# Optimization experiments

Hardware: AMD Instinct MI355X
Metric: run time of the kernel (lower is better)

## Reference

```python
import jax, jax.numpy as jnp
import numpy as np

EPS = 1e-5

def _layernorm(x, g, b):
    mu = jnp.mean(x, axis=-1, keepdims=True)
    var = jnp.mean(jnp.square(x - mu), axis=-1, keepdims=True)
    return (x - mu) * jax.lax.rsqrt(var + EPS) * g + b

def setup_inputs() -> dict:
    key = jax.random.key(0)
    ks = jax.random.split(key, 4)
    E, B, D, H = 8, 131072, 128, 128
    features = jax.random.normal(ks[0], (E, B, D), dtype=jnp.float32)
    gate_w1 = jax.random.normal(ks[1], (E * D, H), dtype=jnp.float32) * (1.0 / np.sqrt(E * D))
    gate_b1 = jnp.zeros((H,), dtype=jnp.float32)
    ln1_g = jnp.ones((H,), dtype=jnp.float32)
    ln1_b = jnp.zeros((H,), dtype=jnp.float32)
    gate_w2 = jax.random.normal(ks[2], (H, E), dtype=jnp.float32) * (1.0 / np.sqrt(H))
    gate_b2 = jnp.zeros((E,), dtype=jnp.float32)
    out_g = jnp.ones((D,), dtype=jnp.float32)
    out_b = jnp.zeros((D,), dtype=jnp.float32)
    return {"features": features, "gate_w1": gate_w1, "gate_b1": gate_b1,
            "ln1_g": ln1_g, "ln1_b": ln1_b, "gate_w2": gate_w2, "gate_b2": gate_b2,
            "out_g": out_g, "out_b": out_b}

def reference(features, gate_w1, gate_b1, ln1_g, ln1_b, gate_w2, gate_b2, out_g, out_b):
    # features: [E, B, D]
    E, B, D = features.shape
    # concat teacher features per sample -> [B, E*D]
    concat = jnp.transpose(features, (1, 0, 2)).reshape(B, E * D)
    h = concat @ gate_w1 + gate_b1                       # [B, 128]
    h = jax.nn.gelu(h, approximate=False)                # torch nn.GELU default = exact
    h = _layernorm(h, ln1_g, ln1_b)
    logits = h @ gate_w2 + gate_b2                       # [B, E]
    scores = jax.nn.softmax(logits, axis=-1)             # [B, E]
    # per-expert scalar weight then LayerNorm over D
    weighted = scores.T[:, :, None] * features           # [E, B, D]
    out = _layernorm(weighted, out_g, out_b)             # [E, B, D]
    return out
```

## Files before the change

### kernel.cpp

```cpp
#include <hip/hip_runtime.h>
#include <hip/hip_bf16.h>

#define B_N   131072
#define E_N   8
#define D_N   128
#define H_N   128
#define K_N   1024
#define MBLK  32
#define NTHR  512

typedef __attribute__((ext_vector_type(8))) short bf16x8;
typedef __attribute__((ext_vector_type(4))) float f32x4;
typedef __attribute__((ext_vector_type(4))) unsigned short u16x4;

__device__ __forceinline__ unsigned short f2bf(float f) {
    union { float f; unsigned int i; } c; c.f = f;
    unsigned int x = c.i;
    return (unsigned short)((x + 0x7fffu + ((x >> 16) & 1u)) >> 16);
}
__device__ __forceinline__ float bf2f(unsigned short u) {
    union { unsigned int i; float f; } c; c.i = ((unsigned int)u) << 16; return c.f;
}

__global__ void prep_w1_frags(const float* __restrict__ w1,
                              unsigned short* __restrict__ frag) {
    int t    = blockIdx.x * blockDim.x + threadIdx.x;
    int lane = t & 63;
    int fgi  = t >> 6;
    int kst  = fgi >> 3;
    int nt   = fgi & 7;
    int n    = nt * 16 + (lane & 15);
    int k0   = kst * 32 + (lane >> 4) * 8;
    bf16x8 v;
    #pragma unroll
    for (int j = 0; j < 8; ++j)
        v[j] = (short)f2bf(w1[(k0 + j) * H_N + n]);
    *reinterpret_cast<bf16x8*>(frag + (size_t)t * 8) = v;
}

__global__ __launch_bounds__(NTHR, 4)
void moe_fused(const float* __restrict__ feats,
               const unsigned short* __restrict__ w1frag,
               const float* __restrict__ gate_b1,
               const float* __restrict__ ln1_g,
               const float* __restrict__ ln1_b,
               const float* __restrict__ gate_w2,
               const float* __restrict__ gate_b2,
               const float* __restrict__ out_g,
               const float* __restrict__ out_b,
               float* __restrict__ out)
{
    __shared__ __attribute__((aligned(16))) unsigned short featS[MBLK * K_N];
    __shared__ __attribute__((aligned(16))) unsigned short hSb[MBLK * 136];
    __shared__ float scoreS[MBLK * E_N];

    const int tid = threadIdx.x;
    const int b0  = blockIdx.x * MBLK;

    #pragma unroll
    for (int i = 0; i < 2; ++i) {
        const int f  = tid + i * NTHR;
        const int m  = f >> 5;
        const int dq = f & 31;
        f32x4 v0 = reinterpret_cast<const f32x4*>(feats + ((size_t)0 * B_N + b0) * D_N)[f];
        f32x4 v1 = reinterpret_cast<const f32x4*>(feats + ((size_t)1 * B_N + b0) * D_N)[f];
        f32x4 v2 = reinterpret_cast<const f32x4*>(feats + ((size_t)2 * B_N + b0) * D_N)[f];
        f32x4 v3 = reinterpret_cast<const f32x4*>(feats + ((size_t)3 * B_N + b0) * D_N)[f];
        f32x4 v4 = reinterpret_cast<const f32x4*>(feats + ((size_t)4 * B_N + b0) * D_N)[f];
        f32x4 v5 = reinterpret_cast<const f32x4*>(feats + ((size_t)5 * B_N + b0) * D_N)[f];
        f32x4 v6 = reinterpret_cast<const f32x4*>(feats + ((size_t)6 * B_N + b0) * D_N)[f];
        f32x4 v7 = reinterpret_cast<const f32x4*>(feats + ((size_t)7 * B_N + b0) * D_N)[f];
        const int sw = (m & 7);
        const int mb = m * K_N;
        #pragma unroll
        for (int e = 0; e < 8; ++e) {
            f32x4 v = (e == 0) ? v0 : (e == 1) ? v1 : (e == 2) ? v2 : (e == 3) ? v3
                    : (e == 4) ? v4 : (e == 5) ? v5 : (e == 6) ? v6 : v7;
            int k    = e * D_N + dq * 4;
            int uoff = mb + ((((k >> 3) ^ sw) << 3) | (k & 7));
            u16x4 u;
            u[0] = f2bf(v[0]); u[1] = f2bf(v[1]);
            u[2] = f2bf(v[2]); u[3] = f2bf(v[3]);
            *reinterpret_cast<u16x4*>(&featS[uoff]) = u;
        }
    }
    __syncthreads();

    const int wv   = tid >> 6;
    const int lane = tid & 63;
    const int lrow = lane & 15;
    const int lkh  = lane >> 4;
    const int rt   = wv >> 2;
    const int nq   = wv & 3;
    const int nt0  = nq * 2, nt1 = nt0 + 1;
    f32x4 acc0 = {0.f, 0.f, 0.f, 0.f};
    f32x4 acc1 = {0.f, 0.f, 0.f, 0.f};
    const bf16x8* wf = reinterpret_cast<const bf16x8*>(w1frag);
    const int arow = (rt * 16 + lrow) * K_N;
    const int asw  = lrow & 7;
    bf16x8 b0c = wf[((0 * 8 + nt0) << 6) + lane];
    bf16x8 b1c = wf[((0 * 8 + nt1) << 6) + lane];
    #pragma unroll
    for (int kk = 0; kk < 32; ++kk) {
        bf16x8 b0n, b1n;
        if (kk < 31) {
            b0n = wf[(((kk + 1) * 8 + nt0) << 6) + lane];
            b1n = wf[(((kk + 1) * 8 + nt1) << 6) + lane];
        }
        bf16x8 a = *reinterpret_cast<const bf16x8*>(
            &featS[arow + ((((kk << 2) + lkh) ^ asw) << 3)]);
        acc0 = __builtin_amdgcn_mfma_f32_16x16x32_bf16(a, b0c, acc0, 0, 0, 0);
        acc1 = __builtin_amdgcn_mfma_f32_16x16x32_bf16(a, b1c, acc1, 0, 0, 0);
        b0c = b0n; b1c = b1n;
    }

    {
        const int colA = nt0 * 16 + lrow;
        const int colB = nt1 * 16 + lrow;
        const float bA = gate_b1[colA];
        const float bB = gate_b1[colB];
        #pragma unroll
        for (int r = 0; r < 4; ++r) {
            int row  = rt * 16 + lkh * 4 + r;
            float vA = acc0[r] + bA;
            float vB = acc1[r] + bB;
            vA = 0.5f * vA * (1.f + erff(vA * 0.70710678118654752f));
            vB = 0.5f * vB * (1.f + erff(vB * 0.70710678118654752f));
            hSb[row * 136 + colA] = f2bf(vA);
            hSb[row * 136 + colB] = f2bf(vB);
        }
    }
    __syncthreads();

    {
        const int row = tid >> 4;
        const int gl  = tid & 15;
        bf16x8 h8 = *reinterpret_cast<const bf16x8*>(&hSb[row * 136 + gl * 8]);
        float hv[8];
        #pragma unroll
        for (int j = 0; j < 8; ++j) hv[j] = bf2f((unsigned short)h8[j]);
        float s = 0.f, sq = 0.f;
        #pragma unroll
        for (int j = 0; j < 8; ++j) { s += hv[j]; sq += hv[j] * hv[j]; }
        #pragma unroll
        for (int msk = 1; msk < 16; msk <<= 1) {
            s  += __shfl_xor(s, msk);
            sq += __shfl_xor(sq, msk);
        }
        float mu  = s * (1.f / 128.f);
        float var = sq * (1.f / 128.f) - mu * mu;
        float rs  = rsqrtf(var + 1e-5f);
        const f32x4* lgv = reinterpret_cast<const f32x4*>(ln1_g + gl * 8);
        const f32x4* lbv = reinterpret_cast<const f32x4*>(ln1_b + gl * 8);
        f32x4 lg0 = lgv[0], lg1 = lgv[1];
        f32x4 lb0 = lbv[0], lb1 = lbv[1];
        float p[8] = {0.f, 0.f, 0.f, 0.f, 0.f, 0.f, 0.f, 0.f};
        #pragma unroll
        for (int j = 0; j < 8; ++j) {
            int col  = gl * 8 + j;
            float g  = (j < 4) ? lg0[j & 3] : lg1[j & 3];
            float bb = (j < 4) ? lb0[j & 3] : lb1[j & 3];
            float hn = (hv[j] - mu) * rs * g + bb;
            const f32x4* w2v = reinterpret_cast<const f32x4*>(gate_w2 + col * 8);
            f32x4 wa = w2v[0], wb = w2v[1];
            #pragma unroll
            for (int e = 0; e < 4; ++e) p[e]     += hn * wa[e];
            #pragma unroll
            for (int e = 0; e < 4; ++e) p[e + 4] += hn * wb[e];
        }
        #pragma unroll
        for (int msk = 1; msk < 16; msk <<= 1) {
            #pragma unroll
            for (int e = 0; e < 8; ++e) p[e] += __shfl_xor(p[e], msk);
        }
        float lg[8], mx = -3.0e38f;
        #pragma unroll
        for (int e = 0; e < 8; ++e) { lg[e] = p[e] + gate_b2[e]; mx = fmaxf(mx, lg[e]); }
        float den = 0.f, ex[8];
        #pragma unroll
        for (int e = 0; e < 8; ++e) { ex[e] = __expf(lg[e] - mx); den += ex[e]; }
        float inv = 1.f / den;
        if (gl < 8) scoreS[row * 8 + gl] = ex[gl] * inv;
    }
    __syncthreads();

    {
        const int m  = tid >> 4;
        const int gl = tid & 15;
        const f32x4* ogv = reinterpret_cast<const f32x4*>(out_g + gl * 8);
        const f32x4* obv = reinterpret_cast<const f32x4*>(out_b + gl * 8);
        f32x4 og0 = ogv[0], og1 = ogv[1];
        f32x4 ob0 = obv[0], ob1 = obv[1];
        #pragma unroll
        for (int e = 0; e < E_N; ++e) {
            int slot = ((e << 4) | gl) ^ (m & 7);
            bf16x8 x8 = *reinterpret_cast<const bf16x8*>(&featS[m * K_N + (slot << 3)]);
            float x[8];
            #pragma unroll
            for (int j = 0; j < 8; ++j) x[j] = bf2f((unsigned short)x8[j]);
            float s = 0.f, sq = 0.f;
            #pragma unroll
            for (int j = 0; j < 8; ++j) { s += x[j]; sq += x[j] * x[j]; }
            #pragma unroll
            for (int msk = 1; msk < 16; msk <<= 1) {
                s  += __shfl_xor(s, msk);
                sq += __shfl_xor(sq, msk);
            }
            float mu  = s * (1.f / 128.f);
            float var = sq * (1.f / 128.f) - mu * mu;
            float sc  = scoreS[m * 8 + e];
            float srs = sc * rsqrtf(sc * sc * var + 1e-5f);
            float* dst = out + ((size_t)e * B_N + b0 + m) * D_N + gl * 8;
            f32x4 o0, o1;
            #pragma unroll
            for (int j = 0; j < 4; ++j)
                o0[j] = (x[j] - mu) * srs * og0[j] + ob0[j];
            #pragma unroll
            for (int j = 0; j < 4; ++j)
                o1[j] = (x[4 + j] - mu) * srs * og1[j] + ob1[j];
            *reinterpret_cast<f32x4*>(dst)     = o0;
            *reinterpret_cast<f32x4*>(dst + 4) = o1;
        }
    }
}

extern "C" void kernel_launch(void* const* d_in, const int* in_sizes, int n_in,
                              void* d_out, int out_size, void* d_ws, size_t ws_size,
                              hipStream_t stream) {
    const float* feats   = (const float*)d_in[0];
    const float* gate_w1 = (const float*)d_in[1];
    const float* gate_b1 = (const float*)d_in[2];
    const float* ln1_g   = (const float*)d_in[3];
    const float* ln1_b   = (const float*)d_in[4];
    const float* gate_w2 = (const float*)d_in[5];
    const float* gate_b2 = (const float*)d_in[6];
    const float* out_g   = (const float*)d_in[7];
    const float* out_b   = (const float*)d_in[8];
    float* outp = (float*)d_out;
    unsigned short* frag = (unsigned short*)d_ws;

    prep_w1_frags<<<64, 256, 0, stream>>>(gate_w1, frag);
    moe_fused<<<B_N / MBLK, NTHR, 0, stream>>>(
        feats, frag, gate_b1, ln1_g, ln1_b, gate_w2, gate_b2, out_g, out_b, outp);
}
```

Before: 303.9 us.

## Make fused gate kernel persistent with register prefetch of next tile

Switches to a persistent grid of 1024 blocks of 256 threads, each looping over 16-row tiles. The next tile's features are loaded into registers while the GEMM epilogue and gating run, hiding global load latency. Output LayerNorm statistics are now computed in a separate pass split across threads and stored in shared memory, so the final write phase is simpler. The cost is many more live registers (64 floats of prefetch per thread), which may lower occupancy, plus extra barriers per tile.

```diff
diff --git a/kernel.cpp b/kernel.cpp
--- a/kernel.cpp
+++ b/kernel.cpp
@@ -6,8 +6,11 @@
 #define D_N   128
 #define H_N   128
 #define K_N   1024
-#define MBLK  32
-#define NTHR  512
+#define MBLK  16
+#define NTHR  256
+#define GRID  1024
+#define TILES (B_N / MBLK)
+#define TPB   (TILES / GRID)
 
 typedef __attribute__((ext_vector_type(8))) short bf16x8;
 typedef __attribute__((ext_vector_type(4))) float f32x4;
@@ -52,155 +55,149 @@
 {
     __shared__ __attribute__((aligned(16))) unsigned short featS[MBLK * K_N];
     __shared__ __attribute__((aligned(16))) unsigned short hSb[MBLK * 136];
-    __shared__ float scoreS[MBLK * E_N];
-
-    const int tid = threadIdx.x;
-    const int b0  = blockIdx.x * MBLK;
-
-    #pragma unroll
-    for (int i = 0; i < 2; ++i) {
-        const int f  = tid + i * NTHR;
-        const int m  = f >> 5;
-        const int dq = f & 31;
-        f32x4 v0 = reinterpret_cast<const f32x4*>(feats + ((size_t)0 * B_N + b0) * D_N)[f];
-        f32x4 v1 = reinterpret_cast<const f32x4*>(feats + ((size_t)1 * B_N + b0) * D_N)[f];
-        f32x4 v2 = reinterpret_cast<const f32x4*>(feats + ((size_t)2 * B_N + b0) * D_N)[f];
-        f32x4 v3 = reinterpret_cast<const f32x4*>(feats + ((size_t)3 * B_N + b0) * D_N)[f];
-        f32x4 v4 = reinterpret_cast<const f32x4*>(feats + ((size_t)4 * B_N + b0) * D_N)[f];
-        f32x4 v5 = reinterpret_cast<const f32x4*>(feats + ((size_t)5 * B_N + b0) * D_N)[f];
-        f32x4 v6 = reinterpret_cast<const f32x4*>(feats + ((size_t)6 * B_N + b0) * D_N)[f];
-        f32x4 v7 = reinterpret_cast<const f32x4*>(feats + ((size_t)7 * B_N + b0) * D_N)[f];
-        const int sw = (m & 7);
-        const int mb = m * K_N;
-        #pragma unroll
-        for (int e = 0; e < 8; ++e) {
-            f32x4 v = (e == 0) ? v0 : (e == 1) ? v1 : (e == 2) ? v2 : (e == 3) ? v3
-                    : (e == 4) ? v4 : (e == 5) ? v5 : (e == 6) ? v6 : v7;
-            int k    = e * D_N + dq * 4;
-            int uoff = mb + ((((k >> 3) ^ sw) << 3) | (k & 7));
-            u16x4 u;
-            u[0] = f2bf(v[0]); u[1] = f2bf(v[1]);
-            u[2] = f2bf(v[2]); u[3] = f2bf(v[3]);
-            *reinterpret_cast<u16x4*>(&featS[uoff]) = u;
-        }
-    }
-    __syncthreads();
+    __shared__ float statSumS[MBLK * E_N];
+    __shared__ float statSqS [MBLK * E_N];
+    __shared__ float muS     [MBLK * E_N];
+    __shared__ float srsS    [MBLK * E_N];
+
+    const int tid  = threadIdx.x;
+    const int bid  = blockIdx.x;
+    const int lane = tid & 63;
+
+    const int m0  = tid >> 5,         dq0 = tid & 31;
+    const int m1  = (tid + NTHR) >> 5, dq1 = (tid + NTHR) & 31;
+    const f32x4 og0 = *reinterpret_cast<const f32x4*>(out_g + dq0 * 4);
+    const f32x4 ob0 = *reinterpret_cast<const f32x4*>(out_b + dq0 * 4);
+    const f32x4 og1 = *reinterpret_cast<const f32x4*>(out_g + dq1 * 4);
+    const f32x4 ob1 = *reinterpret_cast<const f32x4*>(out_b + dq1 * 4);
 
     const int wv   = tid >> 6;
-    const int lane = tid & 63;
     const int lrow = lane & 15;
     const int lkh  = lane >> 4;
-    const int rt   = wv >> 2;
-    const int nq   = wv & 3;
-    const int nt0  = nq * 2, nt1 = nt0 + 1;
-    f32x4 acc0 = {0.f, 0.f, 0.f, 0.f};
-    f32x4 acc1 = {0.f, 0.f, 0.f, 0.f};
+    const int nt0  = wv * 2, nt1 = nt0 + 1;
+    const int arow = lrow * K_N;
+    const int asw  = lrow & 7;
     const bf16x8* wf = reinterpret_cast<const bf16x8*>(w1frag);
-    const int arow = (rt * 16 + lrow) * K_N;
-    const int asw  = lrow & 7;
-    bf16x8 b0c = wf[((0 * 8 + nt0) << 6) + lane];
-    bf16x8 b1c = wf[((0 * 8 + nt1) << 6) + lane];
-    #pragma unroll
-    for (int kk = 0; kk < 32; ++kk) {
-        bf16x8 b0n, b1n;
-        if (kk < 31) {
-            b0n = wf[(((kk + 1) * 8 + nt0) << 6) + lane];
-            b1n = wf[(((kk + 1) * 8 + nt1) << 6) + lane];
-        }
-        bf16x8 a = *reinterpret_cast<const bf16x8*>(
-            &featS[arow + ((((kk << 2) + lkh) ^ asw) << 3)]);
-        acc0 = __builtin_amdgcn_mfma_f32_16x16x32_bf16(a, b0c, acc0, 0, 0, 0);
-        acc1 = __builtin_amdgcn_mfma_f32_16x16x32_bf16(a, b1c, acc1, 0, 0, 0);
-        b0c = b0n; b1c = b1n;
+
+    f32x4 pv0[8], pv1[8];
+
+    {
+        const size_t base = (size_t)bid * MBLK * D_N;
+        #pragma unroll
+        for (int e = 0; e < 8; ++e)
+            pv0[e] = reinterpret_cast<const f32x4*>(feats + (size_t)e * B_N * D_N + base)[tid];
+        #pragma unroll
+        for (int e = 0; e < 8; ++e)
+            pv1[e] = reinterpret_cast<const f32x4*>(feats + (size_t)e * B_N * D_N + base)[tid + NTHR];
     }
 
-    {
-        const int colA = nt0 * 16 + lrow;
-        const int colB = nt1 * 16 + lrow;
-        const float bA = gate_b1[colA];
-        const float bB = gate_b1[colB];
-        #pragma unroll
-        for (int r = 0; r < 4; ++r) {
-            int row  = rt * 16 + lkh * 4 + r;
-            float vA = acc0[r] + bA;
-            float vB = acc1[r] + bB;
-            vA = 0.5f * vA * (1.f + erff(vA * 0.70710678118654752f));
-            vB = 0.5f * vB * (1.f + erff(vB * 0.70710678118654752f));
-            hSb[row * 136 + colA] = f2bf(vA);
-            hSb[row * 136 + colB] = f2bf(vB);
-        }
-    }
-    __syncthreads();
-
-    {
-        const int row = tid >> 4;
-        const int gl  = tid & 15;
-        bf16x8 h8 = *reinterpret_cast<const bf16x8*>(&hSb[row * 136 + gl * 8]);
-        float hv[8];
-        #pragma unroll
-        for (int j = 0; j < 8; ++j) hv[j] = bf2f((unsigned short)h8[j]);
-        float s = 0.f, sq = 0.f;
-        #pragma unroll
-        for (int j = 0; j < 8; ++j) { s += hv[j]; sq += hv[j] * hv[j]; }
-        #pragma unroll
-        for (int msk = 1; msk < 16; msk <<= 1) {
-            s  += __shfl_xor(s, msk);
-            sq += __shfl_xor(sq, msk);
-        }
-        float mu  = s * (1.f / 128.f);
-        float var = sq * (1.f / 128.f) - mu * mu;
-        float rs  = rsqrtf(var + 1e-5f);
-        const f32x4* lgv = reinterpret_cast<const f32x4*>(ln1_g + gl * 8);
-        const f32x4* lbv = reinterpret_cast<const f32x4*>(ln1_b + gl * 8);
-        f32x4 lg0 = lgv[0], lg1 = lgv[1];
-        f32x4 lb0 = lbv[0], lb1 = lbv[1];
-        float p[8] = {0.f, 0.f, 0.f, 0.f, 0.f, 0.f, 0.f, 0.f};
-        #pragma unroll
-        for (int j = 0; j < 8; ++j) {
-            int col  = gl * 8 + j;
-            float g  = (j < 4) ? lg0[j & 3] : lg1[j & 3];
-            float bb = (j < 4) ? lb0[j & 3] : lb1[j & 3];
-            float hn = (hv[j] - mu) * rs * g + bb;
-            const f32x4* w2v = reinterpret_cast<const f32x4*>(gate_w2 + col * 8);
-            f32x4 wa = w2v[0], wb = w2v[1];
-            #pragma unroll
-            for (int e = 0; e < 4; ++e) p[e]     += hn * wa[e];
-            #pragma unroll
-            for (int e = 0; e < 4; ++e) p[e + 4] += hn * wb[e];
-        }
-        #pragma unroll
-        for (int msk = 1; msk < 16; msk <<= 1) {
-            #pragma unroll
-            for (int e = 0; e < 8; ++e) p[e] += __shfl_xor(p[e], msk);
-        }
-        float lg[8], mx = -3.0e38f;
-        #pragma unroll
-        for (int e = 0; e < 8; ++e) { lg[e] = p[e] + gate_b2[e]; mx = fmaxf(mx, lg[e]); }
-        float den = 0.f, ex[8];
-        #pragma unroll
-        for (int e = 0; e < 8; ++e) { ex[e] = __expf(lg[e] - mx); den += ex[e]; }
-        float inv = 1.f / den;
-        if (gl < 8) scoreS[row * 8 + gl] = ex[gl] * inv;
-    }
-    __syncthreads();
-
-    {
-        const int m  = tid >> 4;
-        const int gl = tid & 15;
-        const f32x4* ogv = reinterpret_cast<const f32x4*>(out_g + gl * 8);
-        const f32x4* obv = reinterpret_cast<const f32x4*>(out_b + gl * 8);
-        f32x4 og0 = ogv[0], og1 = ogv[1];
-        f32x4 ob0 = obv[0], ob1 = obv[1];
-        #pragma unroll
-        for (int e = 0; e < E_N; ++e) {
-            int slot = ((e << 4) | gl) ^ (m & 7);
-            bf16x8 x8 = *reinterpret_cast<const bf16x8*>(&featS[m * K_N + (slot << 3)]);
-            float x[8];
-            #pragma unroll
-            for (int j = 0; j < 8; ++j) x[j] = bf2f((unsigned short)x8[j]);
+    for (int g = 0; g < TPB; ++g) {
+        const size_t b0 = (size_t)(g * GRID + bid) * MBLK;
+
+        __syncthreads();
+
+        #pragma unroll
+        for (int i = 0; i < 2; ++i) {
+            const int m  = i ? m1 : m0;
+            const int dq = i ? dq1 : dq0;
+            const int sw = m & 7;
+            const int mb = m * K_N;
+            #pragma unroll
+            for (int e = 0; e < 8; ++e) {
+                f32x4 v = i ? pv1[e] : pv0[e];
+                int k    = e * D_N + dq * 4;
+                int uoff = mb + ((((k >> 3) ^ sw) << 3) | (k & 7));
+                u16x4 u;
+                u[0] = f2bf(v[0]); u[1] = f2bf(v[1]);
+                u[2] = f2bf(v[2]); u[3] = f2bf(v[3]);
+                *reinterpret_cast<u16x4*>(&featS[uoff]) = u;
+            }
+        }
+        __syncthreads();
+
+        {
+            const int r  = tid >> 1;
+            const int h  = tid & 1;
+            const int m  = r >> 3;
+            const int e  = r & 7;
+            const int sw = m & 7;
+            const int mb = m * K_N;
+            const int rot = tid & 7;
             float s = 0.f, sq = 0.f;
             #pragma unroll
-            for (int j = 0; j < 8; ++j) { s += x[j]; sq += x[j] * x[j]; }
+            for (int q = 0; q < 8; ++q) {
+                int k3 = e * 16 + h * 8 + (q ^ rot);
+                bf16x8 x8 = *reinterpret_cast<const bf16x8*>(&featS[mb + ((k3 ^ sw) << 3)]);
+                #pragma unroll
+                for (int j = 0; j < 8; ++j) {
+                    float x = bf2f((unsigned short)x8[j]);
+                    s += x; sq += x * x;
+                }
+            }
+            s  += __shfl_xor(s, 1);
+            sq += __shfl_xor(sq, 1);
+            if (h == 0) { statSumS[r] = s; statSqS[r] = sq; }
+        }
+
+        f32x4 acc0 = {0.f, 0.f, 0.f, 0.f};
+        f32x4 acc1 = {0.f, 0.f, 0.f, 0.f};
+        {
+            bf16x8 b0c = wf[((0 * 8 + nt0) << 6) + lane];
+            bf16x8 b1c = wf[((0 * 8 + nt1) << 6) + lane];
+            #pragma unroll
+            for (int kk = 0; kk < 32; ++kk) {
+                bf16x8 b0n, b1n;
+                if (kk < 31) {
+                    b0n = wf[(((kk + 1) * 8 + nt0) << 6) + lane];
+                    b1n = wf[(((kk + 1) * 8 + nt1) << 6) + lane];
+                }
+                bf16x8 a = *reinterpret_cast<const bf16x8*>(
+                    &featS[arow + ((((kk << 2) + lkh) ^ asw) << 3)]);
+                acc0 = __builtin_amdgcn_mfma_f32_16x16x32_bf16(a, b0c, acc0, 0, 0, 0);
+                acc1 = __builtin_amdgcn_mfma_f32_16x16x32_bf16(a, b1c, acc1, 0, 0, 0);
+                b0c = b0n; b1c = b1n;
+            }
+        }
+
+        __builtin_amdgcn_sched_barrier(0);
+        if (g + 1 < TPB) {
+            const size_t basen = ((size_t)(g + 1) * GRID + bid) * MBLK * D_N;
+            #pragma unroll
+            for (int e = 0; e < 8; ++e)
+                pv0[e] = reinterpret_cast<const f32x4*>(feats + (size_t)e * B_N * D_N + basen)[tid];
+            #pragma unroll
+            for (int e = 0; e < 8; ++e)
+                pv1[e] = reinterpret_cast<const f32x4*>(feats + (size_t)e * B_N * D_N + basen)[tid + NTHR];
+        }
+
+        {
+            const int colA = nt0 * 16 + lrow;
+            const int colB = nt1 * 16 + lrow;
+            const float bA = gate_b1[colA];
+            const float bB = gate_b1[colB];
+            #pragma unroll
+            for (int r = 0; r < 4; ++r) {
+                int row  = lkh * 4 + r;
+                float vA = acc0[r] + bA;
+                float vB = acc1[r] + bB;
+                vA = 0.5f * vA * (1.f + erff(vA * 0.70710678118654752f));
+                vB = 0.5f * vB * (1.f + erff(vB * 0.70710678118654752f));
+                hSb[row * 136 + colA] = f2bf(vA);
+                hSb[row * 136 + colB] = f2bf(vB);
+            }
+        }
+        __syncthreads();
+
+        {
+            const int row = tid >> 4;
+            const int gl  = tid & 15;
+            bf16x8 h8 = *reinterpret_cast<const bf16x8*>(&hSb[row * 136 + gl * 8]);
+            float hv[8];
+            #pragma unroll
+            for (int j = 0; j < 8; ++j) hv[j] = bf2f((unsigned short)h8[j]);
+            float s = 0.f, sq = 0.f;
+            #pragma unroll
+            for (int j = 0; j < 8; ++j) { s += hv[j]; sq += hv[j] * hv[j]; }
             #pragma unroll
             for (int msk = 1; msk < 16; msk <<= 1) {
                 s  += __shfl_xor(s, msk);
@@ -208,18 +205,71 @@
             }
             float mu  = s * (1.f / 128.f);
             float var = sq * (1.f / 128.f) - mu * mu;
-            float sc  = scoreS[m * 8 + e];
-            float srs = sc * rsqrtf(sc * sc * var + 1e-5f);
-            float* dst = out + ((size_t)e * B_N + b0 + m) * D_N + gl * 8;
-            f32x4 o0, o1;
-            #pragma unroll
-            for (int j = 0; j < 4; ++j)
-                o0[j] = (x[j] - mu) * srs * og0[j] + ob0[j];
-            #pragma unroll
-            for (int j = 0; j < 4; ++j)
-                o1[j] = (x[4 + j] - mu) * srs * og1[j] + ob1[j];
-            *reinterpret_cast<f32x4*>(dst)     = o0;
-            *reinterpret_cast<f32x4*>(dst + 4) = o1;
+            float rs  = rsqrtf(var + 1e-5f);
+            const f32x4* lgv = reinterpret_cast<const f32x4*>(ln1_g + gl * 8);
+            const f32x4* lbv = reinterpret_cast<const f32x4*>(ln1_b + gl * 8);
+            f32x4 lg0 = lgv[0], lg1 = lgv[1];
+            f32x4 lb0 = lbv[0], lb1 = lbv[1];
+            float p[8] = {0.f, 0.f, 0.f, 0.f, 0.f, 0.f, 0.f, 0.f};
+            #pragma unroll
+            for (int j = 0; j < 8; ++j) {
+                int col  = gl * 8 + j;
+                float gg = (j < 4) ? lg0[j & 3] : lg1[j & 3];
+                float bb = (j < 4) ? lb0[j & 3] : lb1[j & 3];
+                float hn = (hv[j] - mu) * rs * gg + bb;
+                const f32x4* w2v = reinterpret_cast<const f32x4*>(gate_w2 + col * 8);
+                f32x4 wa = w2v[0], wb = w2v[1];
+                #pragma unroll
+                for (int e = 0; e < 4; ++e) p[e]     += hn * wa[e];
+                #pragma unroll
+                for (int e = 0; e < 4; ++e) p[e + 4] += hn * wb[e];
+            }
+            #pragma unroll
+            for (int msk = 1; msk < 16; msk <<= 1) {
+                #pragma unroll
+                for (int e = 0; e < 8; ++e) p[e] += __shfl_xor(p[e], msk);
+            }
+            float lg[8], mx = -3.0e38f;
+            #pragma unroll
+            for (int e = 0; e < 8; ++e) { lg[e] = p[e] + gate_b2[e]; mx = fmaxf(mx, lg[e]); }
+            float den = 0.f, ex[8];
+            #pragma unroll
+            for (int e = 0; e < 8; ++e) { ex[e] = __expf(lg[e] - mx); den += ex[e]; }
+            float inv = 1.f / den;
+            if (gl < 8) {
+                int r = row * 8 + gl;
+                float sc   = ex[gl] * inv;
+                float ss   = statSumS[r], qq = statSqS[r];
+                float mu2  = ss * (1.f / 128.f);
+                float var2 = qq * (1.f / 128.f) - mu2 * mu2;
+                float srs  = sc * rsqrtf(sc * sc * var2 + 1e-5f);
+                muS[r]  = mu2;
+                srsS[r] = srs;
+            }
+        }
+        __syncthreads();
+
+        #pragma unroll
+        for (int i = 0; i < 2; ++i) {
+            const int m  = i ? m1 : m0;
+            const int dq = i ? dq1 : dq0;
+            const int sw = m & 7;
+            const int mb = m * K_N;
+            const f32x4 og = i ? og1 : og0;
+            const f32x4 ob = i ? ob1 : ob0;
+            #pragma unroll
+            for (int e = 0; e < 8; ++e) {
+                int k3  = e * 16 + (dq >> 1);
+                int off = mb + (((k3 ^ sw) << 3) | ((dq & 1) << 2));
+                u16x4 xb = *reinterpret_cast<const u16x4*>(&featS[off]);
+                int r = m * 8 + e;
+                float mu = muS[r], srs = srsS[r];
+                f32x4 o;
+                #pragma unroll
+                for (int j = 0; j < 4; ++j)
+                    o[j] = (bf2f(xb[j]) - mu) * srs * og[j] + ob[j];
+                *reinterpret_cast<f32x4*>(out + ((size_t)e * B_N + b0 + m) * D_N + dq * 4) = o;
+            }
         }
     }
 }
@@ -240,6 +290,6 @@
     unsigned short* frag = (unsigned short*)d_ws;
 
     prep_w1_frags<<<64, 256, 0, stream>>>(gate_w1, frag);
-    moe_fused<<<B_N / MBLK, NTHR, 0, stream>>>(
+    moe_fused<<<GRID, NTHR, 0, stream>>>(
         feats, frag, gate_b1, ln1_g, ln1_b, gate_w2, gate_b2, out_g, out_b, outp);
 }
```

After: 1.206 ms. 3.97x slower.
